# Optimization experiments

Hardware: AMD Instinct MI355X
Metric: run time of the kernel (lower is better)

## Reference

```python
import jax, jax.numpy as jnp
import numpy as np

M = 500000  # inner reduction dim per group; 4 groups x 21 outputs = 84 rows of tmp


def setup_inputs() -> dict:
    key = jax.random.key(0)
    ks = jax.random.split(key, 5)
    probs_params = jnp.array([
        [1.8134, 1.6573, -0.2452, 1.8745],
        [2.6430, 1.5442, -0.0449, 1.5576],
        [2.8379, 1.4989, 0.0158, 1.4974],
        [2.9666, 1.4671, 0.0577, 1.4586],
        [3.0934, 1.4350, 0.1002, 1.4213],
    ], dtype=jnp.float32)
    return {
        "BEV": jax.random.normal(ks[0], (1,), jnp.float32),
        "ST0": jax.random.normal(ks[1], (4, M), jnp.float32),
        "Weight0": jax.random.normal(ks[2], (4, M, 21), jnp.float32),
        "ST1": jax.random.normal(ks[3], (4, M), jnp.float32),
        "Weight1": jax.random.normal(ks[4], (4, M, 21), jnp.float32),
        "probs_params": probs_params,          # the 5 probsK nn.Parameters stacked
        "BEV_p": jnp.float32(0.2058),           # self.BEV parameter
        "B": jnp.float32(0.3089),               # self.B parameter
    }


def calc_probs(p):
    # p: softmaxed 4-vector. Reproduces the nested-loop ordering:
    # for i: [p_i, for j: [p_i*p_j, for k: p_i*p_j*p_k]] -> 84 entries.
    o2 = p[:, None] * p[None, :]                  # (4,4)   p_i*p_j
    o3 = o2[:, :, None] * p[None, None, :]        # (4,4,4) p_i*p_j*p_k
    block = jnp.concatenate([o2[:, :, None], o3], axis=2)       # (4,4,5)
    per_i = jnp.concatenate([p[:, None], block.reshape(4, 20)], axis=1)  # (4,21)
    return per_i.reshape(-1)                      # (84,)


def reference(BEV, ST0, Weight0, ST1, Weight1, probs_params, BEV_p, B):
    # (5,84) -- calc_probs of softmax of each of the 5 parameter vectors
    P = jax.vmap(calc_probs)(jax.nn.softmax(probs_params, axis=-1))
    base = jax.nn.relu(BEV_p) * BEV[0]            # scalar, broadcast over ST
    sig0 = jax.nn.sigmoid(B * (base + ST0))       # (4, M)
    sig1 = jax.nn.sigmoid(B * (base + ST1))       # (4, M)
    # per-group matvec sigmoid(.) @ Weight[i], concatenated -> (84,)
    tmp0 = jnp.einsum('im,imp->ip', sig0, Weight0).reshape(-1)
    tmp1 = jnp.einsum('im,imp->ip', sig1, Weight1).reshape(-1)
    outs = jnp.concatenate([(P[0] @ tmp0)[None], P[1:] @ tmp1])  # (5,)
    return jnp.mean(outs)
```

## Files before the change

kernel.cpp:

```cpp
#include <hip/hip_runtime.h>
#include <hip/hip_bf16.h>

#define M_DIM 500000
#define NPER  21
#define NELEM (M_DIM * NPER)
#define NF4   (NELEM / 4)
#define NBLK  256
#define TPB   252

__device__ __forceinline__ float sigmoidf(float x) {
    return 1.0f / (1.0f + __expf(-x));
}

__global__ __launch_bounds__(TPB) void probs_reduce_kernel(
    const float* __restrict__ ST0, const float* __restrict__ W0,
    const float* __restrict__ ST1, const float* __restrict__ W1,
    const float* __restrict__ BEV, const float* __restrict__ BEVp,
    const float* __restrict__ Bp, float* __restrict__ tmp)
{
    const int t   = threadIdx.x;
    const int tau = blockIdx.y >> 2;
    const int grp = blockIdx.y & 3;

    const float* ST = (tau == 0 ? ST0 : ST1) + grp * M_DIM;
    const float4* W = (const float4*)((tau == 0 ? W0 : W1) + (size_t)grp * NELEM);

    const float B    = Bp[0];
    const float base = fmaxf(BEVp[0], 0.0f) * BEV[0];

    const int g0 = blockIdx.x * TPB + t;
    const int S  = NBLK * TPB;

    float acc0 = 0.f, acc1 = 0.f, acc2 = 0.f, acc3 = 0.f;

    for (int f = g0; f < NF4; f += S) {
        float4 w = W[f];
        int e0 = f * 4;
        int m0 = (int)((unsigned)e0 / 21u);
        int r  = e0 - m0 * 21;
        int m1 = m0 + 1; if (m1 >= M_DIM) m1 = M_DIM - 1;
        float s0 = sigmoidf(B * (base + ST[m0]));
        float s1 = sigmoidf(B * (base + ST[m1]));
        acc0 += w.x * ((r + 0 < 21) ? s0 : s1);
        acc1 += w.y * ((r + 1 < 21) ? s0 : s1);
        acc2 += w.z * ((r + 2 < 21) ? s0 : s1);
        acc3 += w.w * ((r + 3 < 21) ? s0 : s1);
    }

    __shared__ float sm[TPB * 4];
    sm[t * 4 + 0] = acc0;
    sm[t * 4 + 1] = acc1;
    sm[t * 4 + 2] = acc2;
    sm[t * 4 + 3] = acc3;
    __syncthreads();

    if (t < NPER) {
        float s = 0.f;
        #pragma unroll
        for (int q = 0; q < (TPB * 4) / NPER; ++q)
            s += sm[t + NPER * q];
        atomicAdd(&tmp[blockIdx.y * NPER + t], s);
    }
}

__global__ void probs_final_kernel(const float* __restrict__ tmp,
                                   const float* __restrict__ pp,
                                   float* __restrict__ out)
{
    __shared__ float red[128];
    const int t = threadIdx.x;
    float val = 0.f;
    if (t < 84) {
        const int i = t / 21, inner = t % 21;
        float Pk[5];
        #pragma unroll
        for (int k = 0; k < 5; ++k) {
            float a0 = pp[k*4+0], a1 = pp[k*4+1], a2 = pp[k*4+2], a3 = pp[k*4+3];
            float mx = fmaxf(fmaxf(a0, a1), fmaxf(a2, a3));
            float e0 = __expf(a0-mx), e1 = __expf(a1-mx), e2 = __expf(a2-mx), e3 = __expf(a3-mx);
            float inv = 1.0f / (e0 + e1 + e2 + e3);
            float q0 = e0*inv, q1 = e1*inv, q2 = e2*inv, q3 = e3*inv;
            float q[4] = {q0, q1, q2, q3};
            float v = q[i];
            if (inner > 0) {
                int jj = (inner - 1) / 5, kk = (inner - 1) % 5;
                v *= q[jj];
                if (kk > 0) v *= q[kk - 1];
            }
            Pk[k] = v;
        }
        float t0 = tmp[t], t1 = tmp[84 + t];
        val = Pk[0] * t0 + (Pk[1] + Pk[2] + Pk[3] + Pk[4]) * t1;
    }
    red[t] = val;
    __syncthreads();
    #pragma unroll
    for (int s = 64; s > 0; s >>= 1) {
        if (t < s) red[t] += red[t + s];
        __syncthreads();
    }
    if (t == 0) out[0] = red[0] * 0.2f;
}

extern "C" void kernel_launch(void* const* d_in, const int* in_sizes, int n_in,
                              void* d_out, int out_size, void* d_ws, size_t ws_size,
                              hipStream_t stream) {
    const float* BEV  = (const float*)d_in[0];
    const float* ST0  = (const float*)d_in[1];
    const float* W0   = (const float*)d_in[2];
    const float* ST1  = (const float*)d_in[3];
    const float* W1   = (const float*)d_in[4];
    const float* pp   = (const float*)d_in[5];
    const float* BEVp = (const float*)d_in[6];
    const float* B    = (const float*)d_in[7];
    float* out = (float*)d_out;
    float* tmp = (float*)d_ws;

    hipMemsetAsync(tmp, 0, 168 * sizeof(float), stream);
    probs_reduce_kernel<<<dim3(NBLK, 8), TPB, 0, stream>>>(ST0, W0, ST1, W1,
                                                           BEV, BEVp, B, tmp);
    probs_final_kernel<<<1, 128, 0, stream>>>(tmp, pp, out);
}
```

Before: 74.89 us.

## Software-pipeline the weight stream with loop-invariant row offsets and fast sigmoid

Each thread now loads two float4 weight vectors per step. The stride is chosen so that the row index advances by a constant and the column remainder stays fixed, which removes the per-iteration integer division and lane-select recomputation. The next iteration's weights and ST values are prefetched before the current step's math, with a sched_barrier to keep the loads ahead. Sigmoid is computed with exp2 and rcp builtins using precomputed constants. These changes aim to hide memory latency in this bandwidth-bound reduction, at the cost of more registers and a fixed iteration count tied to the problem size.

```diff
diff --git a/kernel.cpp b/kernel.cpp
--- a/kernel.cpp
+++ b/kernel.cpp
@@ -1,15 +1,19 @@
 #include <hip/hip_runtime.h>
 #include <hip/hip_bf16.h>
 
-#define M_DIM 500000
-#define NPER  21
-#define NELEM (M_DIM * NPER)
-#define NF4   (NELEM / 4)
-#define NBLK  256
-#define TPB   252
+#define M_DIM   500000
+#define NPER    21
+#define NELEM   (M_DIM * NPER)
+#define NF4     (NELEM / 4)
+#define NBLK    256
+#define TPB     252
+#define CH      2
+#define STR_F4  (NBLK * TPB * CH)
+#define DM      ((STR_F4 * 4) / 21)
+#define FULLP   20
 
-__device__ __forceinline__ float sigmoidf(float x) {
-    return 1.0f / (1.0f + __expf(-x));
+__device__ __forceinline__ float sig_fast(float st, float k1, float k0) {
+    return __builtin_amdgcn_rcpf(1.0f + __builtin_amdgcn_exp2f(fmaf(st, k1, k0)));
 }
 
 __global__ __launch_bounds__(TPB) void probs_reduce_kernel(
@@ -22,42 +26,74 @@
     const int tau = blockIdx.y >> 2;
     const int grp = blockIdx.y & 3;
 
-    const float* ST = (tau == 0 ? ST0 : ST1) + grp * M_DIM;
-    const float4* W = (const float4*)((tau == 0 ? W0 : W1) + (size_t)grp * NELEM);
+    const float* __restrict__ ST = (tau == 0 ? ST0 : ST1) + grp * M_DIM;
+    const float4* __restrict__ W = (const float4*)((tau == 0 ? W0 : W1) + (size_t)grp * NELEM);
 
     const float B    = Bp[0];
     const float base = fmaxf(BEVp[0], 0.0f) * BEV[0];
+    const float k1   = -B * 1.44269504f;
+    const float k0   = k1 * base;
 
-    const int g0 = blockIdx.x * TPB + t;
-    const int S  = NBLK * TPB;
+    int c0 = (blockIdx.x * TPB + t) * CH;
+    const int e0 = c0 * 4;
+    int m = (int)((unsigned)e0 / 21u);
+    const int cthr = 21 - (e0 - m * 21);
 
-    float acc0 = 0.f, acc1 = 0.f, acc2 = 0.f, acc3 = 0.f;
+    float a0=0.f,a1=0.f,a2=0.f,a3=0.f,a4=0.f,a5=0.f,a6=0.f,a7=0.f;
 
-    for (int f = g0; f < NF4; f += S) {
-        float4 w = W[f];
-        int e0 = f * 4;
-        int m0 = (int)((unsigned)e0 / 21u);
-        int r  = e0 - m0 * 21;
-        int m1 = m0 + 1; if (m1 >= M_DIM) m1 = M_DIM - 1;
-        float s0 = sigmoidf(B * (base + ST[m0]));
-        float s1 = sigmoidf(B * (base + ST[m1]));
-        acc0 += w.x * ((r + 0 < 21) ? s0 : s1);
-        acc1 += w.y * ((r + 1 < 21) ? s0 : s1);
-        acc2 += w.z * ((r + 2 < 21) ? s0 : s1);
-        acc3 += w.w * ((r + 3 < 21) ? s0 : s1);
+    float4 wA = W[c0], wB = W[c0 + 1];
+    float  s0 = ST[m];
+    int    mp = (m + 1 < M_DIM) ? m + 1 : M_DIM - 1;
+    float  s1 = ST[mp];
+
+    #pragma unroll 1
+    for (int p = 0; p < FULLP; ++p) {
+        const int cn = c0 + STR_F4;
+        const int mn = m + DM;
+        const bool v = (cn < NF4);
+        const int cv = v ? cn : 0;
+        const int mv = v ? mn : m;
+        float4 nA = W[cv], nB = W[cv + 1];
+        float  n0 = ST[mv];
+        int    mq = (mv + 1 < M_DIM) ? mv + 1 : M_DIM - 1;
+        float  n1 = ST[mq];
+        __builtin_amdgcn_sched_barrier(0);
+
+        const float g0 = sig_fast(s0, k1, k0);
+        const float g1 = sig_fast(s1, k1, k0);
+        a0 = fmaf(wA.x, g0, a0);
+        a1 = fmaf(wA.y, (1 < cthr) ? g0 : g1, a1);
+        a2 = fmaf(wA.z, (2 < cthr) ? g0 : g1, a2);
+        a3 = fmaf(wA.w, (3 < cthr) ? g0 : g1, a3);
+        a4 = fmaf(wB.x, (4 < cthr) ? g0 : g1, a4);
+        a5 = fmaf(wB.y, (5 < cthr) ? g0 : g1, a5);
+        a6 = fmaf(wB.z, (6 < cthr) ? g0 : g1, a6);
+        a7 = fmaf(wB.w, (7 < cthr) ? g0 : g1, a7);
+
+        wA = nA; wB = nB; s0 = n0; s1 = n1; c0 = cn; m = mn;
+    }
+    if (c0 < NF4) {
+        const float g0 = sig_fast(s0, k1, k0);
+        const float g1 = sig_fast(s1, k1, k0);
+        a0 = fmaf(wA.x, g0, a0);
+        a1 = fmaf(wA.y, (1 < cthr) ? g0 : g1, a1);
+        a2 = fmaf(wA.z, (2 < cthr) ? g0 : g1, a2);
+        a3 = fmaf(wA.w, (3 < cthr) ? g0 : g1, a3);
+        a4 = fmaf(wB.x, (4 < cthr) ? g0 : g1, a4);
+        a5 = fmaf(wB.y, (5 < cthr) ? g0 : g1, a5);
+        a6 = fmaf(wB.z, (6 < cthr) ? g0 : g1, a6);
+        a7 = fmaf(wB.w, (7 < cthr) ? g0 : g1, a7);
     }
 
-    __shared__ float sm[TPB * 4];
-    sm[t * 4 + 0] = acc0;
-    sm[t * 4 + 1] = acc1;
-    sm[t * 4 + 2] = acc2;
-    sm[t * 4 + 3] = acc3;
+    __shared__ float sm[TPB * 8];
+    sm[t*8+0]=a0; sm[t*8+1]=a1; sm[t*8+2]=a2; sm[t*8+3]=a3;
+    sm[t*8+4]=a4; sm[t*8+5]=a5; sm[t*8+6]=a6; sm[t*8+7]=a7;
     __syncthreads();
 
     if (t < NPER) {
         float s = 0.f;
         #pragma unroll
-        for (int q = 0; q < (TPB * 4) / NPER; ++q)
+        for (int q = 0; q < (TPB * 8) / NPER; ++q)
             s += sm[t + NPER * q];
         atomicAdd(&tmp[blockIdx.y * NPER + t], s);
     }
@@ -79,8 +115,7 @@
             float mx = fmaxf(fmaxf(a0, a1), fmaxf(a2, a3));
             float e0 = __expf(a0-mx), e1 = __expf(a1-mx), e2 = __expf(a2-mx), e3 = __expf(a3-mx);
             float inv = 1.0f / (e0 + e1 + e2 + e3);
-            float q0 = e0*inv, q1 = e1*inv, q2 = e2*inv, q3 = e3*inv;
-            float q[4] = {q0, q1, q2, q3};
+            float q[4] = {e0*inv, e1*inv, e2*inv, e3*inv};
             float v = q[i];
             if (inner > 0) {
                 int jj = (inner - 1) / 5, kk = (inner - 1) % 5;
```

New measurement: 73.82 us. No clear change (-1.4%).

## Tile weight stream per block with shared sigmoid table and asm-pipelined loads

Applied to the files above, without the earlier changes.

Each block now owns a contiguous chunk of Weight and first computes the sigmoid values for the rows it covers once into shared memory. It then streams its chunk with hand-issued global_load_dwordx4 pairs kept DEPTH passes ahead, using explicit vmcnt waits. This removes the per-element integer division, the redundant ST loads and sigmoid evaluations, and aims to keep more loads in flight. The cost is more register pressure from the 21-entry unrolled load arrays and fragile inline asm waitcnt bookkeeping.

```diff
diff --git a/kernel.cpp b/kernel.cpp
--- a/kernel.cpp
+++ b/kernel.cpp
@@ -1,15 +1,27 @@
 #include <hip/hip_runtime.h>
 #include <hip/hip_bf16.h>
 
-#define M_DIM 500000
-#define NPER  21
-#define NELEM (M_DIM * NPER)
-#define NF4   (NELEM / 4)
-#define NBLK  256
-#define TPB   252
+typedef float f32x4 __attribute__((ext_vector_type(4)));
 
-__device__ __forceinline__ float sigmoidf(float x) {
-    return 1.0f / (1.0f + __expf(-x));
+#define M_DIM   500000
+#define NPER    21
+#define NELEM   (M_DIM * NPER)
+#define TPB     252
+#define PASS_E  (TPB * 8)
+#define NPASS   21
+#define BLK_E   (PASS_E * NPASS)
+#define NFULL   248
+#define NBLKX   249
+#define TBL     (BLK_E / NPER + 1)
+#define DEPTH   4
+
+#define ISSUE2(loz, hiz, ap)                                            \
+    asm volatile("global_load_dwordx4 %0, %2, off\n\t"                  \
+                 "global_load_dwordx4 %1, %2, off offset:16"            \
+                 : "=&v"(loz), "=&v"(hiz) : "v"(ap))
+
+__device__ __forceinline__ float sig_fast(float st, float k1, float k0) {
+    return __builtin_amdgcn_rcpf(1.0f + __builtin_amdgcn_exp2f(fmaf(st, k1, k0)));
 }
 
 __global__ __launch_bounds__(TPB) void probs_reduce_kernel(
@@ -18,47 +30,97 @@
     const float* __restrict__ BEV, const float* __restrict__ BEVp,
     const float* __restrict__ Bp, float* __restrict__ tmp)
 {
+    __shared__ float smem[TBL];
     const int t   = threadIdx.x;
+    const int b   = blockIdx.x;
     const int tau = blockIdx.y >> 2;
     const int grp = blockIdx.y & 3;
 
-    const float* ST = (tau == 0 ? ST0 : ST1) + grp * M_DIM;
-    const float4* W = (const float4*)((tau == 0 ? W0 : W1) + (size_t)grp * NELEM);
+    const float* __restrict__ ST = (tau == 0 ? ST0 : ST1) + grp * M_DIM;
+    const float* __restrict__ Wg = (tau == 0 ? W0 : W1) + (size_t)grp * NELEM;
 
     const float B    = Bp[0];
     const float base = fmaxf(BEVp[0], 0.0f) * BEV[0];
+    const float k1   = -B * 1.44269504f;
+    const float k0   = k1 * base;
 
-    const int g0 = blockIdx.x * TPB + t;
-    const int S  = NBLK * TPB;
+    const int m_base = b * (BLK_E / NPER);
+    for (int i = t; i < TBL; i += TPB) {
+        int mi = m_base + i;
+        if (mi > M_DIM - 1) mi = M_DIM - 1;
+        smem[i] = sig_fast(ST[mi], k1, k0);
+    }
+    __syncthreads();
 
-    float acc0 = 0.f, acc1 = 0.f, acc2 = 0.f, acc3 = 0.f;
+    float a0=0.f,a1=0.f,a2=0.f,a3=0.f,a4=0.f,a5=0.f,a6=0.f,a7=0.f;
+    const int r0   = (t * 8) % 21;
+    const int cthr = 21 - r0;
+    const int ml0  = (t * 8) / 21;
 
-    for (int f = g0; f < NF4; f += S) {
-        float4 w = W[f];
-        int e0 = f * 4;
-        int m0 = (int)((unsigned)e0 / 21u);
-        int r  = e0 - m0 * 21;
-        int m1 = m0 + 1; if (m1 >= M_DIM) m1 = M_DIM - 1;
-        float s0 = sigmoidf(B * (base + ST[m0]));
-        float s1 = sigmoidf(B * (base + ST[m1]));
-        acc0 += w.x * ((r + 0 < 21) ? s0 : s1);
-        acc1 += w.y * ((r + 1 < 21) ? s0 : s1);
-        acc2 += w.z * ((r + 2 < 21) ? s0 : s1);
-        acc3 += w.w * ((r + 3 < 21) ? s0 : s1);
+    if (b < NFULL) {
+        const float* tb = Wg + (size_t)b * BLK_E + t * 8;
+        f32x4 lo[NPASS], hi[NPASS];
+
+        #pragma unroll
+        for (int s = 0; s < DEPTH; ++s) {
+            const float* ap = tb + s * PASS_E;
+            ISSUE2(lo[s], hi[s], ap);
+        }
+
+        #pragma unroll
+        for (int s = 0; s < NPASS; ++s) {
+            if (s + DEPTH < NPASS) {
+                const float* ap = tb + (s + DEPTH) * PASS_E;
+                ISSUE2(lo[s + DEPTH], hi[s + DEPTH], ap);
+            }
+            const int im = (s + DEPTH < NPASS) ? s + DEPTH : NPASS - 1;
+            const int vm = 2 * (im - s);
+            if      (vm >= 8) asm volatile("s_waitcnt vmcnt(8)" ::: "memory");
+            else if (vm == 6) asm volatile("s_waitcnt vmcnt(6)" ::: "memory");
+            else if (vm == 4) asm volatile("s_waitcnt vmcnt(4)" ::: "memory");
+            else if (vm == 2) asm volatile("s_waitcnt vmcnt(2)" ::: "memory");
+            else              asm volatile("s_waitcnt vmcnt(0)" ::: "memory");
+            __builtin_amdgcn_sched_barrier(0);
+
+            const int   ml = ml0 + 96 * s;
+            const float gA = smem[ml];
+            const float gB = smem[ml + 1];
+            const f32x4 L = lo[s], H = hi[s];
+            a0 = fmaf(L[0], gA, a0);
+            a1 = fmaf(L[1], (1 < cthr) ? gA : gB, a1);
+            a2 = fmaf(L[2], (2 < cthr) ? gA : gB, a2);
+            a3 = fmaf(L[3], (3 < cthr) ? gA : gB, a3);
+            a4 = fmaf(H[0], (4 < cthr) ? gA : gB, a4);
+            a5 = fmaf(H[1], (5 < cthr) ? gA : gB, a5);
+            a6 = fmaf(H[2], (6 < cthr) ? gA : gB, a6);
+            a7 = fmaf(H[3], (7 < cthr) ? gA : gB, a7);
+        }
+    } else if (t < (NELEM - NFULL * BLK_E) / 8) {
+        const float* tb = Wg + (size_t)NFULL * BLK_E + t * 8;
+        const f32x4 L = *(const f32x4*)tb;
+        const f32x4 H = *(const f32x4*)(tb + 4);
+        const float gA = smem[ml0];
+        const float gB = smem[ml0 + 1];
+        a0 = fmaf(L[0], gA, a0);
+        a1 = fmaf(L[1], (1 < cthr) ? gA : gB, a1);
+        a2 = fmaf(L[2], (2 < cthr) ? gA : gB, a2);
+        a3 = fmaf(L[3], (3 < cthr) ? gA : gB, a3);
+        a4 = fmaf(H[0], (4 < cthr) ? gA : gB, a4);
+        a5 = fmaf(H[1], (5 < cthr) ? gA : gB, a5);
+        a6 = fmaf(H[2], (6 < cthr) ? gA : gB, a6);
+        a7 = fmaf(H[3], (7 < cthr) ? gA : gB, a7);
     }
 
-    __shared__ float sm[TPB * 4];
-    sm[t * 4 + 0] = acc0;
-    sm[t * 4 + 1] = acc1;
-    sm[t * 4 + 2] = acc2;
-    sm[t * 4 + 3] = acc3;
+    __syncthreads();
+    smem[t*8+0]=a0; smem[t*8+1]=a1; smem[t*8+2]=a2; smem[t*8+3]=a3;
+    smem[t*8+4]=a4; smem[t*8+5]=a5; smem[t*8+6]=a6; smem[t*8+7]=a7;
     __syncthreads();
 
     if (t < NPER) {
         float s = 0.f;
         #pragma unroll
-        for (int q = 0; q < (TPB * 4) / NPER; ++q)
-            s += sm[t + NPER * q];
+        for (int q = 0; q < (TPB * 8) / NPER; ++q)
+            s += smem[t + NPER * q];
         atomicAdd(&tmp[blockIdx.y * NPER + t], s);
     }
 }
@@ -79,8 +141,7 @@
             float mx = fmaxf(fmaxf(a0, a1), fmaxf(a2, a3));
             float e0 = __expf(a0-mx), e1 = __expf(a1-mx), e2 = __expf(a2-mx), e3 = __expf(a3-mx);
             float inv = 1.0f / (e0 + e1 + e2 + e3);
-            float q0 = e0*inv, q1 = e1*inv, q2 = e2*inv, q3 = e3*inv;
-            float q[4] = {q0, q1, q2, q3};
+            float q[4] = {e0*inv, e1*inv, e2*inv, e3*inv};
             float v = q[i];
             if (inner > 0) {
                 int jj = (inner - 1) / 5, kk = (inner - 1) % 5;
@@ -117,7 +178,7 @@
     float* tmp = (float*)d_ws;
 
     hipMemsetAsync(tmp, 0, 168 * sizeof(float), stream);
-    probs_reduce_kernel<<<dim3(NBLK, 8), TPB, 0, stream>>>(ST0, W0, ST1, W1,
-                                                           BEV, BEVp, B, tmp);
+    probs_reduce_kernel<<<dim3(NBLKX, 8), TPB, 0, stream>>>(ST0, W0, ST1, W1,
+                                                            BEV, BEVp, B, tmp);
     probs_final_kernel<<<1, 128, 0, stream>>>(tmp, pp, out);
 }
```

Measured after the change: 81.92 us. 1.09x slower.
